# Optimization experiments

Measured on AMD Instinct MI355X. Metric: run time of the kernel, lower is better.

Reference implementation:

```python
import jax, jax.numpy as jnp
import numpy as np

T = 4        # number of atom types (len(atomtype))
N = 65536    # number of atoms
D = 256      # nl[0] == nl[1] == nl[2]
EPS = 1e-5   # LayerNorm eps (torch default)


def setup_inputs() -> dict:
    key = jax.random.key(0)
    ks = jax.random.split(key, 16)
    s = 1.0 / np.sqrt(D)  # xavier-ish scale
    f32 = jnp.float32
    return {
        "density": jax.random.normal(ks[0], (N, D), f32),
        "species": jax.random.randint(ks[1], (N,), 0, T, jnp.int32),
        # first Linear(nl[0], nl[1]) per type
        "W0": jax.random.normal(ks[2], (T, D, D), f32) * s,
        "b0": jnp.zeros((T, D), f32),
        # ResBlock: actfun (Relu_like: alpha*silu(Wx+b)), LayerNorm, Linear
        "Wa": jax.random.normal(ks[3], (T, D, D), f32) * s,
        "ba": jnp.zeros((T, D), f32),
        "alpha_a": jnp.ones((T, D), f32),
        "gamma": jnp.ones((T, D), f32),
        "beta_ln": jnp.zeros((T, D), f32),
        "Wl": jax.random.normal(ks[4], (T, D, D), f32) * s,
        "bl": jnp.zeros((T, D), f32),
        # tail actfun(nl[nhid-1], nl[nhid])
        "Wf": jax.random.normal(ks[5], (T, D, D), f32) * s,
        "bf": jnp.zeros((T, D), f32),
        "alpha_f": jnp.ones((T, D), f32),
        # output Linear(nl[nhid], outputneuron=1); randomized (zero-init is degenerate for testing)
        "Wo": jax.random.normal(ks[6], (T, 1, D), f32) * s,
        "bo": jnp.zeros((T, 1), f32),
    }


def _layernorm(x, g, b):
    mu = jnp.mean(x, axis=-1, keepdims=True)
    var = jnp.mean((x - mu) ** 2, axis=-1, keepdims=True)
    return g * (x - mu) * jax.lax.rsqrt(var + EPS) + b


def _expert(W0, b0, Wa, ba, alpha_a, gamma, beta_ln, Wl, bl, Wf, bf, alpha_f, Wo, bo, density):
    # Sequential: Linear -> ResBlock(actfun, LN, Linear) -> actfun -> Linear
    x = density @ W0.T + b0                       # [N, D]
    h = alpha_a * jax.nn.silu(x @ Wa.T + ba)      # Relu_like actfun
    h = _layernorm(h, gamma, beta_ln)
    x = x + (h @ Wl.T + bl)                       # residual add
    x = alpha_f * jax.nn.silu(x @ Wf.T + bf)
    return x @ Wo.T + bo                          # [N, 1]


def reference(density, species, W0, b0, Wa, ba, alpha_a, gamma, beta_ln, Wl, bl, Wf, bf, alpha_f, Wo, bo):
    # Apply every type's expert to all atoms, then pick the row for each atom's type.
    # Same math as the torch gather/scatter dispatch (every species value is in [0, T)).
    y_all = jax.vmap(_expert, in_axes=(0,) * 14 + (None,))(
        W0, b0, Wa, ba, alpha_a, gamma, beta_ln, Wl, bl, Wf, bf, alpha_f, Wo, bo, density
    )  # [T, N, 1]
    return y_all[species, jnp.arange(N)]          # [N, 1]
```

## Files before the change

### kernel.cpp

```cpp
#include <hip/hip_runtime.h>
#include <hip/hip_bf16.h>


#define D 256
#define T 4
#define MT 64
#define NTHREADS 512
#define CSTRIDE 32

#define XSW(row, col) (((row) << 8) + ((col) ^ (((row) & 7) << 3)))

typedef __attribute__((ext_vector_type(8))) short bf16x8;
typedef __attribute__((ext_vector_type(4))) float f32x4;

__device__ __forceinline__ float bf2f(unsigned short s) {
    union { unsigned u; float f; } c;
    c.u = ((unsigned)s) << 16;
    return c.f;
}
__device__ __forceinline__ unsigned cvtpk(float a, float b) {
    unsigned r;
    asm("v_cvt_pk_bf16_f32 %0, %1, %2" : "=v"(r) : "v"(a), "v"(b));
    return r;
}
__device__ __forceinline__ float lo2f(unsigned u) { return bf2f((unsigned short)(u & 0xffffu)); }
__device__ __forceinline__ float hi2f(unsigned u) { return bf2f((unsigned short)(u >> 16)); }
__device__ __forceinline__ float silu(float v) {
    return v * __builtin_amdgcn_rcpf(1.f + __expf(-v));
}

__device__ __forceinline__ void barrier_lds() {
    __builtin_amdgcn_sched_barrier(0);
    asm volatile("s_waitcnt lgkmcnt(0)" ::: "memory");
    __builtin_amdgcn_s_barrier();
    __builtin_amdgcn_sched_barrier(0);
}

extern "C" __global__ void k_prep(const int* __restrict__ species, int* cursors,
                                  int* __restrict__ perm, int N,
                                  const float* __restrict__ s0, const float* __restrict__ s1,
                                  const float* __restrict__ s2, const float* __restrict__ s3,
                                  unsigned short* __restrict__ d0, unsigned short* __restrict__ d1,
                                  unsigned short* __restrict__ d2, unsigned short* __restrict__ d3, int n4) {
    __shared__ int lh[T], lbase[T];
    int tid = threadIdx.x;
    if (tid < T) lh[tid] = 0;
    __syncthreads();
    int i = blockIdx.x * blockDim.x + tid;
    int t = -1, rank = 0;
    if (i < N) {
        t = species[i];
        rank = atomicAdd(&lh[t], 1);
    }
    if (i < n4) {
        float4 v;
        v = ((const float4*)s0)[i]; ((uint2*)d0)[i] = make_uint2(cvtpk(v.x, v.y), cvtpk(v.z, v.w));
        v = ((const float4*)s1)[i]; ((uint2*)d1)[i] = make_uint2(cvtpk(v.x, v.y), cvtpk(v.z, v.w));
        v = ((const float4*)s2)[i]; ((uint2*)d2)[i] = make_uint2(cvtpk(v.x, v.y), cvtpk(v.z, v.w));
        v = ((const float4*)s3)[i]; ((uint2*)d3)[i] = make_uint2(cvtpk(v.x, v.y), cvtpk(v.z, v.w));
    }
    __syncthreads();
    if (tid < T) lbase[tid] = atomicAdd(&cursors[tid * CSTRIDE], lh[tid]);
    __syncthreads();
    if (t >= 0) perm[t * N + lbase[t] + rank] = i;
}


extern "C" __global__ void __launch_bounds__(NTHREADS, 4)
fused_moe(const float* __restrict__ density,
          const int* __restrict__ perm,
          const int* __restrict__ counts,
          const unsigned short* __restrict__ W0b,
          const unsigned short* __restrict__ Wab,
          const unsigned short* __restrict__ Wlb,
          const unsigned short* __restrict__ Wfb,
          const float* __restrict__ b0g, const float* __restrict__ bag,
          const float* __restrict__ aag, const float* __restrict__ gg,
          const float* __restrict__ btg, const float* __restrict__ blg,
          const float* __restrict__ bfg, const float* __restrict__ afg,
          const float* __restrict__ Wog, const float* __restrict__ bog,
          float* __restrict__ out, int N)
{
    __shared__ unsigned short Xs[2][MT * D];
    __shared__ float Pb0[D], Pba[D], Paa[D], Pg[D], Pbt[D], Pbl[D], Pbf[D], Paf[D], Pwo[D];
    __shared__ float red1[NTHREADS], red2[NTHREADS];

    const int tid = threadIdx.x;

    const int nwg = gridDim.x;
    const int qq = nwg >> 3, rr = nwg & 7;
    const int xcd = blockIdx.x & 7, lid = blockIdx.x >> 3;
    const int vb = (xcd < rr ? xcd * (qq + 1) : rr * (qq + 1) + (xcd - rr) * qq) + lid;

    int c[T];
#pragma unroll
    for (int i = 0; i < T; ++i) c[i] = counts[i * CSTRIDE];
    int t = -1, tile = 0, rem = vb;
#pragma unroll
    for (int i = 0; i < T; ++i) {
        int ti = (c[i] + MT - 1) >> 6;
        if (t < 0) {
            if (rem < ti) { t = i; tile = rem; }
            else rem -= ti;
        }
    }
    if (t < 0) return;
    const int bstart = t * N + tile * MT;
    const int nrows = min(MT, c[t] - tile * MT);

    const int lane = tid & 63;
    const int w    = tid >> 6;
    const int ml   = lane & 15;
    const int qk   = (lane >> 4) * 8;
    const int qr   = (lane >> 4) * 4;

    const size_t wmat = (size_t)t * D * D;
    const unsigned short* W0t = W0b + wmat;
    const unsigned short* Wat = Wab + wmat;
    const unsigned short* Wlt = Wlb + wmat;
    const unsigned short* Wft = Wfb + wmat;

    bf16x8 abuf[2][4];
    auto prefA = [&](const unsigned short* __restrict__ W) {
#pragma unroll
        for (int p = 0; p < 2; ++p)
#pragma unroll
            for (int s = 0; s < 2; ++s)
#pragma unroll
                for (int mi = 0; mi < 2; ++mi)
                    abuf[p][s * 2 + mi] =
                        *(const bf16x8*)(W + (size_t)(w * 32 + mi * 16 + ml) * D + p * 64 + s * 32 + qk);
    };

    prefA(W0t);

    if (tid < D) {
        int j = t * D + tid;
        Pb0[tid] = b0g[j]; Pba[tid] = bag[j]; Paa[tid] = aag[j];
        Pg[tid]  = gg[j];  Pbt[tid] = btg[j]; Pbl[tid] = blg[j];
        Pbf[tid] = bfg[j]; Paf[tid] = afg[j]; Pwo[tid] = Wog[j];
    }

#pragma unroll
    for (int p = 0; p < 2; ++p) {
        int row = p * 32 + (tid >> 4);
        int cbase = (tid & 15) * 4;
        if (row < nrows) {
            const float* src = density + (size_t)perm[bstart + row] * D;
#pragma unroll
            for (int j = 0; j < 4; ++j) {
                int col = cbase + j * 64;
                float4 v = *(const float4*)(src + col);
                *(uint2*)(&Xs[0][XSW(row, col)]) = make_uint2(cvtpk(v.x, v.y), cvtpk(v.z, v.w));
            }
        } else {
#pragma unroll
            for (int j = 0; j < 4; ++j)
                *(uint2*)(&Xs[0][XSW(row, cbase + j * 64)]) = make_uint2(0u, 0u);
        }
    }
    barrier_lds();

    f32x4 acc[2][4];
    const f32x4 zero4 = {0.f, 0.f, 0.f, 0.f};

    auto do_gemm = [&](const unsigned short* __restrict__ W, const unsigned short* __restrict__ Xb) {
#pragma unroll
        for (int mi = 0; mi < 2; ++mi)
#pragma unroll
            for (int ni = 0; ni < 4; ++ni) acc[mi][ni] = zero4;
#pragma unroll
        for (int kp = 0; kp < 4; ++kp) {
            const int cur = kp & 1;
#pragma unroll
            for (int s = 0; s < 2; ++s) {
                const int k0 = kp * 64 + s * 32;
                bf16x8 b[4];
#pragma unroll
                for (int ni = 0; ni < 4; ++ni)
                    b[ni] = *(const bf16x8*)(Xb + XSW(ni * 16 + ml, k0 + qk));
#pragma unroll
                for (int mi = 0; mi < 2; ++mi)
#pragma unroll
                    for (int ni = 0; ni < 4; ++ni)
                        acc[mi][ni] = __builtin_amdgcn_mfma_f32_16x16x32_bf16(
                            abuf[cur][s * 2 + mi], b[ni], acc[mi][ni], 0, 0, 0);
                if (kp < 2) {
                    const int kb = (kp + 2) * 64 + s * 32;
#pragma unroll
                    for (int mi = 0; mi < 2; ++mi)
                        abuf[cur][s * 2 + mi] =
                            *(const bf16x8*)(W + (size_t)(w * 32 + mi * 16 + ml) * D + kb + qk);
                }
            }
        }
    };


    do_gemm(W0t, Xs[0]);
    prefA(Wat);
#pragma unroll
    for (int mi = 0; mi < 2; ++mi) {
#pragma unroll
        for (int ni = 0; ni < 4; ++ni) {
            int r0 = w * 32 + mi * 16 + qr;
            int a0 = ni * 16 + ml;
            float4 bb = *(const float4*)(Pb0 + r0);
            unsigned p01 = cvtpk(acc[mi][ni][0] + bb.x, acc[mi][ni][1] + bb.y);
            unsigned p23 = cvtpk(acc[mi][ni][2] + bb.z, acc[mi][ni][3] + bb.w);
            *(uint2*)(&Xs[1][XSW(a0, r0)]) = make_uint2(p01, p23);
        }
    }
    barrier_lds();

    do_gemm(Wat, Xs[1]);
    prefA(Wlt);
#pragma unroll
    for (int mi = 0; mi < 2; ++mi) {
#pragma unroll
        for (int ni = 0; ni < 4; ++ni) {
            int r0 = w * 32 + mi * 16 + qr;
            int a0 = ni * 16 + ml;
            float4 bb = *(const float4*)(Pba + r0);
            float4 aa = *(const float4*)(Paa + r0);
            float v0 = aa.x * silu(acc[mi][ni][0] + bb.x);
            float v1 = aa.y * silu(acc[mi][ni][1] + bb.y);
            float v2 = aa.z * silu(acc[mi][ni][2] + bb.z);
            float v3 = aa.w * silu(acc[mi][ni][3] + bb.w);
            *(uint2*)(&Xs[0][XSW(a0, r0)]) = make_uint2(cvtpk(v0, v1), cvtpk(v2, v3));
        }
    }
    barrier_lds();

    {
        int row = tid & 63, q = tid >> 6;
        bf16x8 hv[4];
        float sum = 0.f, ssq = 0.f;
#pragma unroll
        for (int j = 0; j < 4; ++j) {
            hv[j] = *(const bf16x8*)(&Xs[0][XSW(row, q * 32 + j * 8)]);
#pragma unroll
            for (int e = 0; e < 8; ++e) {
                float f = bf2f((unsigned short)hv[j][e]);
                sum += f;
                ssq = fmaf(f, f, ssq);
            }
        }
        red1[tid] = sum; red2[tid] = ssq;
        barrier_lds();
        if (tid < MT) {
            float s = 0.f, sq = 0.f;
#pragma unroll
            for (int k = 0; k < 8; ++k) { s += red1[tid + 64 * k]; sq += red2[tid + 64 * k]; }
            float mu = s * (1.f / D);
            float var = sq * (1.f / D) - mu * mu;
            red1[tid] = mu;
            red2[tid] = rsqrtf(var + 1e-5f);
        }
        barrier_lds();
        float mu = red1[row], rs = red2[row];
#pragma unroll
        for (int j = 0; j < 4; ++j) {
            float n[8];
#pragma unroll
            for (int e = 0; e < 8; ++e) {
                int col = q * 32 + j * 8 + e;
                float f = bf2f((unsigned short)hv[j][e]);
                n[e] = fmaf((f - mu) * rs, Pg[col], Pbt[col]);
            }
            uint4 o = make_uint4(cvtpk(n[0], n[1]), cvtpk(n[2], n[3]),
                                 cvtpk(n[4], n[5]), cvtpk(n[6], n[7]));
            *(uint4*)(&Xs[0][XSW(row, q * 32 + j * 8)]) = o;
        }
    }
    barrier_lds();

    do_gemm(Wlt, Xs[0]);
    prefA(Wft);
#pragma unroll
    for (int mi = 0; mi < 2; ++mi) {
#pragma unroll
        for (int ni = 0; ni < 4; ++ni) {
            int r0 = w * 32 + mi * 16 + qr;
            int a0 = ni * 16 + ml;
            float4 bb = *(const float4*)(Pbl + r0);
            uint2 old = *(const uint2*)(&Xs[1][XSW(a0, r0)]);
            float v0 = acc[mi][ni][0] + bb.x + lo2f(old.x);
            float v1 = acc[mi][ni][1] + bb.y + hi2f(old.x);
            float v2 = acc[mi][ni][2] + bb.z + lo2f(old.y);
            float v3 = acc[mi][ni][3] + bb.w + hi2f(old.y);
            *(uint2*)(&Xs[1][XSW(a0, r0)]) = make_uint2(cvtpk(v0, v1), cvtpk(v2, v3));
        }
    }
    barrier_lds();

    do_gemm(Wft, Xs[1]);
#pragma unroll
    for (int mi = 0; mi < 2; ++mi) {
#pragma unroll
        for (int ni = 0; ni < 4; ++ni) {
            int r0 = w * 32 + mi * 16 + qr;
            int a0 = ni * 16 + ml;
            float4 bb = *(const float4*)(Pbf + r0);
            float4 aa = *(const float4*)(Paf + r0);
            float v0 = aa.x * silu(acc[mi][ni][0] + bb.x);
            float v1 = aa.y * silu(acc[mi][ni][1] + bb.y);
            float v2 = aa.z * silu(acc[mi][ni][2] + bb.z);
            float v3 = aa.w * silu(acc[mi][ni][3] + bb.w);
            *(uint2*)(&Xs[0][XSW(a0, r0)]) = make_uint2(cvtpk(v0, v1), cvtpk(v2, v3));
        }
    }
    barrier_lds();

    {
        int row = tid & 63, q = tid >> 6;
        float part = 0.f;
#pragma unroll
        for (int j = 0; j < 4; ++j) {
            bf16x8 hv = *(const bf16x8*)(&Xs[0][XSW(row, q * 32 + j * 8)]);
#pragma unroll
            for (int e = 0; e < 8; ++e)
                part = fmaf(bf2f((unsigned short)hv[e]), Pwo[q * 32 + j * 8 + e], part);
        }
        red1[tid] = part;
        barrier_lds();
        if (tid < nrows) {
            float val = bog[t];
#pragma unroll
            for (int k = 0; k < 8; ++k) val += red1[tid + 64 * k];
            out[perm[bstart + tid]] = val;
        }
    }
}


extern "C" void kernel_launch(void* const* d_in, const int* in_sizes, int n_in,
                              void* d_out, int out_size, void* d_ws, size_t ws_size,
                              hipStream_t stream) {
    const float* density = (const float*)d_in[0];
    const int*   species = (const int*)d_in[1];
    const float* W0      = (const float*)d_in[2];
    const float* b0      = (const float*)d_in[3];
    const float* Wa      = (const float*)d_in[4];
    const float* ba      = (const float*)d_in[5];
    const float* alpha_a = (const float*)d_in[6];
    const float* gamma   = (const float*)d_in[7];
    const float* beta_ln = (const float*)d_in[8];
    const float* Wl      = (const float*)d_in[9];
    const float* bl      = (const float*)d_in[10];
    const float* Wf      = (const float*)d_in[11];
    const float* bfv     = (const float*)d_in[12];
    const float* alpha_f = (const float*)d_in[13];
    const float* Wo      = (const float*)d_in[14];
    const float* bo      = (const float*)d_in[15];
    float* out = (float*)d_out;
    const int N = in_sizes[1];

    char* ws = (char*)d_ws;
    int* cursors = (int*)ws;
    int* perm    = (int*)(ws + 1024);
    const size_t wsz = (size_t)T * D * D;
    unsigned short* W0b = (unsigned short*)(ws + 1024 + (size_t)T * N * 4);
    unsigned short* Wab = W0b + wsz;
    unsigned short* Wlb = Wab + wsz;
    unsigned short* Wfb = Wlb + wsz;

    hipMemsetAsync(ws, 0, 512, stream);
    int n4 = (int)(wsz / 4);
    int pb = ((N > n4 ? N : n4) + 255) / 256;
    k_prep<<<pb, 256, 0, stream>>>(species, cursors, perm, N, W0, Wa, Wl, Wf,
                                   W0b, Wab, Wlb, Wfb, n4);

    int nblocks = (N + MT - 1) / MT + T;
    fused_moe<<<nblocks, NTHREADS, 0, stream>>>(density, perm, cursors, W0b, Wab, Wlb, Wfb,
                                                b0, ba, alpha_a, gamma, beta_ln, bl, bfv, alpha_f,
                                                Wo, bo, out, N);
}
```

Measured before the change: 195.0 us.

## Fuse LayerNorm stats and output dot into GEMM epilogues, drop A-prefetch

Computes the LayerNorm sum and sum-of-squares directly from fp32 accumulators in the second GEMM epilogue, reducing them with wave shuffles and a small LDS array. The separate LDS pass that re-read the activations for statistics goes away. The final silu and output dot product are likewise fused into the last GEMM epilogue, which removes one LDS write, a barrier and a read. The double-buffered register prefetch of weight tiles is replaced by a simple per-k load. That lowers register pressure but exposes global or L2 latency inside the GEMM loop.

```diff
diff --git a/kernel.cpp b/kernel.cpp
--- a/kernel.cpp
+++ b/kernel.cpp
@@ -120,20 +120,6 @@
     const unsigned short* Wlt = Wlb + wmat;
     const unsigned short* Wft = Wfb + wmat;
 
-    bf16x8 abuf[2][4];
-    auto prefA = [&](const unsigned short* __restrict__ W) {
-#pragma unroll
-        for (int p = 0; p < 2; ++p)
-#pragma unroll
-            for (int s = 0; s < 2; ++s)
-#pragma unroll
-                for (int mi = 0; mi < 2; ++mi)
-                    abuf[p][s * 2 + mi] =
-                        *(const bf16x8*)(W + (size_t)(w * 32 + mi * 16 + ml) * D + p * 64 + s * 32 + qk);
-    };
-
-    prefA(W0t);
-
     if (tid < D) {
         int j = t * D + tid;
         Pb0[tid] = b0g[j]; Pba[tid] = bag[j]; Paa[tid] = aag[j];
@@ -170,35 +156,25 @@
 #pragma unroll
             for (int ni = 0; ni < 4; ++ni) acc[mi][ni] = zero4;
 #pragma unroll
-        for (int kp = 0; kp < 4; ++kp) {
-            const int cur = kp & 1;
-#pragma unroll
-            for (int s = 0; s < 2; ++s) {
-                const int k0 = kp * 64 + s * 32;
-                bf16x8 b[4];
+        for (int k0 = 0; k0 < D; k0 += 32) {
+            bf16x8 a[2], b[4];
+#pragma unroll
+            for (int mi = 0; mi < 2; ++mi)
+                a[mi] = *(const bf16x8*)(W + (size_t)(w * 32 + mi * 16 + ml) * D + k0 + qk);
+#pragma unroll
+            for (int ni = 0; ni < 4; ++ni)
+                b[ni] = *(const bf16x8*)(Xb + XSW(ni * 16 + ml, k0 + qk));
+#pragma unroll
+            for (int mi = 0; mi < 2; ++mi)
 #pragma unroll
                 for (int ni = 0; ni < 4; ++ni)
-                    b[ni] = *(const bf16x8*)(Xb + XSW(ni * 16 + ml, k0 + qk));
-#pragma unroll
-                for (int mi = 0; mi < 2; ++mi)
-#pragma unroll
-                    for (int ni = 0; ni < 4; ++ni)
-                        acc[mi][ni] = __builtin_amdgcn_mfma_f32_16x16x32_bf16(
-                            abuf[cur][s * 2 + mi], b[ni], acc[mi][ni], 0, 0, 0);
-                if (kp < 2) {
-                    const int kb = (kp + 2) * 64 + s * 32;
-#pragma unroll
-                    for (int mi = 0; mi < 2; ++mi)
-                        abuf[cur][s * 2 + mi] =
-                            *(const bf16x8*)(W + (size_t)(w * 32 + mi * 16 + ml) * D + kb + qk);
-                }
-            }
+                    acc[mi][ni] = __builtin_amdgcn_mfma_f32_16x16x32_bf16(
+                        a[mi], b[ni], acc[mi][ni], 0, 0, 0);
         }
     };
 
 
     do_gemm(W0t, Xs[0]);
-    prefA(Wat);
 #pragma unroll
     for (int mi = 0; mi < 2; ++mi) {
 #pragma unroll
@@ -214,58 +190,64 @@
     barrier_lds();
 
     do_gemm(Wat, Xs[1]);
-    prefA(Wlt);
-#pragma unroll
-    for (int mi = 0; mi < 2; ++mi) {
+    {
+        float psum[4] = {0.f, 0.f, 0.f, 0.f}, pssq[4] = {0.f, 0.f, 0.f, 0.f};
+#pragma unroll
+        for (int mi = 0; mi < 2; ++mi) {
+#pragma unroll
+            for (int ni = 0; ni < 4; ++ni) {
+                int r0 = w * 32 + mi * 16 + qr;
+                int a0 = ni * 16 + ml;
+                float4 bb = *(const float4*)(Pba + r0);
+                float4 aa = *(const float4*)(Paa + r0);
+                float v0 = aa.x * silu(acc[mi][ni][0] + bb.x);
+                float v1 = aa.y * silu(acc[mi][ni][1] + bb.y);
+                float v2 = aa.z * silu(acc[mi][ni][2] + bb.z);
+                float v3 = aa.w * silu(acc[mi][ni][3] + bb.w);
+                psum[ni] += v0 + v1 + v2 + v3;
+                pssq[ni] = fmaf(v0, v0, fmaf(v1, v1, fmaf(v2, v2, fmaf(v3, v3, pssq[ni]))));
+                *(uint2*)(&Xs[0][XSW(a0, r0)]) = make_uint2(cvtpk(v0, v1), cvtpk(v2, v3));
+            }
+        }
 #pragma unroll
         for (int ni = 0; ni < 4; ++ni) {
-            int r0 = w * 32 + mi * 16 + qr;
-            int a0 = ni * 16 + ml;
-            float4 bb = *(const float4*)(Pba + r0);
-            float4 aa = *(const float4*)(Paa + r0);
-            float v0 = aa.x * silu(acc[mi][ni][0] + bb.x);
-            float v1 = aa.y * silu(acc[mi][ni][1] + bb.y);
-            float v2 = aa.z * silu(acc[mi][ni][2] + bb.z);
-            float v3 = aa.w * silu(acc[mi][ni][3] + bb.w);
-            *(uint2*)(&Xs[0][XSW(a0, r0)]) = make_uint2(cvtpk(v0, v1), cvtpk(v2, v3));
-        }
-    }
-    barrier_lds();
-
+            psum[ni] += __shfl_xor(psum[ni], 16, 64);
+            psum[ni] += __shfl_xor(psum[ni], 32, 64);
+            pssq[ni] += __shfl_xor(pssq[ni], 16, 64);
+            pssq[ni] += __shfl_xor(pssq[ni], 32, 64);
+        }
+        if (lane < 16) {
+#pragma unroll
+            for (int ni = 0; ni < 4; ++ni) {
+                int a0 = ni * 16 + lane;
+                red1[a0 * 8 + w] = psum[ni];
+                red2[a0 * 8 + w] = pssq[ni];
+            }
+        }
+    }
+    barrier_lds();
+
+    if (tid < MT) {
+        float s = 0.f, sq = 0.f;
+#pragma unroll
+        for (int k = 0; k < 8; ++k) { s += red1[tid * 8 + k]; sq += red2[tid * 8 + k]; }
+        float mu = s * (1.f / D);
+        float var = sq * (1.f / D) - mu * mu;
+        red1[tid] = mu;
+        red2[tid] = rsqrtf(var + 1e-5f);
+    }
+    barrier_lds();
     {
         int row = tid & 63, q = tid >> 6;
-        bf16x8 hv[4];
-        float sum = 0.f, ssq = 0.f;
+        float mu = red1[row], rs = red2[row];
 #pragma unroll
         for (int j = 0; j < 4; ++j) {
-            hv[j] = *(const bf16x8*)(&Xs[0][XSW(row, q * 32 + j * 8)]);
-#pragma unroll
-            for (int e = 0; e < 8; ++e) {
-                float f = bf2f((unsigned short)hv[j][e]);
-                sum += f;
-                ssq = fmaf(f, f, ssq);
-            }
-        }
-        red1[tid] = sum; red2[tid] = ssq;
-        barrier_lds();
-        if (tid < MT) {
-            float s = 0.f, sq = 0.f;
-#pragma unroll
-            for (int k = 0; k < 8; ++k) { s += red1[tid + 64 * k]; sq += red2[tid + 64 * k]; }
-            float mu = s * (1.f / D);
-            float var = sq * (1.f / D) - mu * mu;
-            red1[tid] = mu;
-            red2[tid] = rsqrtf(var + 1e-5f);
-        }
-        barrier_lds();
-        float mu = red1[row], rs = red2[row];
-#pragma unroll
-        for (int j = 0; j < 4; ++j) {
+            bf16x8 hv = *(const bf16x8*)(&Xs[0][XSW(row, q * 32 + j * 8)]);
             float n[8];
 #pragma unroll
             for (int e = 0; e < 8; ++e) {
                 int col = q * 32 + j * 8 + e;
-                float f = bf2f((unsigned short)hv[j][e]);
+                float f = bf2f((unsigned short)hv[e]);
                 n[e] = fmaf((f - mu) * rs, Pg[col], Pbt[col]);
             }
             uint4 o = make_uint4(cvtpk(n[0], n[1]), cvtpk(n[2], n[3]),
@@ -276,7 +258,6 @@
     barrier_lds();
 
     do_gemm(Wlt, Xs[0]);
-    prefA(Wft);
 #pragma unroll
     for (int mi = 0; mi < 2; ++mi) {
 #pragma unroll
@@ -295,41 +276,41 @@
     barrier_lds();
 
     do_gemm(Wft, Xs[1]);
-#pragma unroll
-    for (int mi = 0; mi < 2; ++mi) {
+    {
+        float pdot[4] = {0.f, 0.f, 0.f, 0.f};
+#pragma unroll
+        for (int mi = 0; mi < 2; ++mi) {
+#pragma unroll
+            for (int ni = 0; ni < 4; ++ni) {
+                int r0 = w * 32 + mi * 16 + qr;
+                float4 bb = *(const float4*)(Pbf + r0);
+                float4 aa = *(const float4*)(Paf + r0);
+                float4 wo = *(const float4*)(Pwo + r0);
+                float v0 = aa.x * silu(acc[mi][ni][0] + bb.x);
+                float v1 = aa.y * silu(acc[mi][ni][1] + bb.y);
+                float v2 = aa.z * silu(acc[mi][ni][2] + bb.z);
+                float v3 = aa.w * silu(acc[mi][ni][3] + bb.w);
+                pdot[ni] = fmaf(v0, wo.x, fmaf(v1, wo.y, fmaf(v2, wo.z, fmaf(v3, wo.w, pdot[ni]))));
+            }
+        }
 #pragma unroll
         for (int ni = 0; ni < 4; ++ni) {
-            int r0 = w * 32 + mi * 16 + qr;
-            int a0 = ni * 16 + ml;
-            float4 bb = *(const float4*)(Pbf + r0);
-            float4 aa = *(const float4*)(Paf + r0);
-            float v0 = aa.x * silu(acc[mi][ni][0] + bb.x);
-            float v1 = aa.y * silu(acc[mi][ni][1] + bb.y);
-            float v2 = aa.z * silu(acc[mi][ni][2] + bb.z);
-            float v3 = aa.w * silu(acc[mi][ni][3] + bb.w);
-            *(uint2*)(&Xs[0][XSW(a0, r0)]) = make_uint2(cvtpk(v0, v1), cvtpk(v2, v3));
-        }
-    }
-    barrier_lds();
-
-    {
-        int row = tid & 63, q = tid >> 6;
-        float part = 0.f;
-#pragma unroll
-        for (int j = 0; j < 4; ++j) {
-            bf16x8 hv = *(const bf16x8*)(&Xs[0][XSW(row, q * 32 + j * 8)]);
-#pragma unroll
-            for (int e = 0; e < 8; ++e)
-                part = fmaf(bf2f((unsigned short)hv[e]), Pwo[q * 32 + j * 8 + e], part);
-        }
-        red1[tid] = part;
-        barrier_lds();
-        if (tid < nrows) {
-            float val = bog[t];
-#pragma unroll
-            for (int k = 0; k < 8; ++k) val += red1[tid + 64 * k];
-            out[perm[bstart + tid]] = val;
-        }
+            pdot[ni] += __shfl_xor(pdot[ni], 16, 64);
+            pdot[ni] += __shfl_xor(pdot[ni], 32, 64);
+        }
+        if (lane < 16) {
+#pragma unroll
+            for (int ni = 0; ni < 4; ++ni)
+                red1[(ni * 16 + lane) * 8 + w] = pdot[ni];
+        }
+    }
+    barrier_lds();
+
+    if (tid < nrows) {
+        float val = bog[t];
+#pragma unroll
+        for (int k = 0; k < 8; ++k) val += red1[tid * 8 + k];
+        out[perm[bstart + tid]] = val;
     }
 }
 
```

Result: slower. 202.7 us (+3.9%).

## Halve row tile to 32 and drop weight register prefetch for higher occupancy

Applied to the files above, without the earlier changes.

The atom tile per block is halved from 64 to 32 rows, so each warp computes a 32x32 output block per GEMM instead of 32x64. The double-buffered register prefetch of weight fragments is removed; weights are now loaded directly inside the k-loop. Launch bounds are raised to allow 6 blocks per CU. The LayerNorm and output-reduction thread mappings are reworked to 16 threads per row. The intent is more blocks and waves in flight to hide latency, at the cost of reading each weight matrix twice as often per atom and losing the explicit global-load overlap.

```diff
diff --git a/kernel.cpp b/kernel.cpp
--- a/kernel.cpp
+++ b/kernel.cpp
@@ -4,7 +4,7 @@
 
 #define D 256
 #define T 4
-#define MT 64
+#define MT 32
 #define NTHREADS 512
 #define CSTRIDE 32
 
@@ -66,7 +66,7 @@
 }
 
 
-extern "C" __global__ void __launch_bounds__(NTHREADS, 4)
+extern "C" __global__ void __launch_bounds__(NTHREADS, 6)
 fused_moe(const float* __restrict__ density,
           const int* __restrict__ perm,
           const int* __restrict__ counts,
@@ -98,7 +98,7 @@
     int t = -1, tile = 0, rem = vb;
 #pragma unroll
     for (int i = 0; i < T; ++i) {
-        int ti = (c[i] + MT - 1) >> 6;
+        int ti = (c[i] + MT - 1) >> 5;
         if (t < 0) {
             if (rem < ti) { t = i; tile = rem; }
             else rem -= ti;
@@ -120,20 +120,6 @@
     const unsigned short* Wlt = Wlb + wmat;
     const unsigned short* Wft = Wfb + wmat;
 
-    bf16x8 abuf[2][4];
-    auto prefA = [&](const unsigned short* __restrict__ W) {
-#pragma unroll
-        for (int p = 0; p < 2; ++p)
-#pragma unroll
-            for (int s = 0; s < 2; ++s)
-#pragma unroll
-                for (int mi = 0; mi < 2; ++mi)
-                    abuf[p][s * 2 + mi] =
-                        *(const bf16x8*)(W + (size_t)(w * 32 + mi * 16 + ml) * D + p * 64 + s * 32 + qk);
-    };
-
-    prefA(W0t);
-
     if (tid < D) {
         int j = t * D + tid;
         Pb0[tid] = b0g[j]; Pba[tid] = bag[j]; Paa[tid] = aag[j];
@@ -141,9 +127,8 @@
         Pbf[tid] = bfg[j]; Paf[tid] = afg[j]; Pwo[tid] = Wog[j];
     }
 
-#pragma unroll
-    for (int p = 0; p < 2; ++p) {
-        int row = p * 32 + (tid >> 4);
+    {
+        int row = tid >> 4;
         int cbase = (tid & 15) * 4;
         if (row < nrows) {
             const float* src = density + (size_t)perm[bstart + row] * D;
@@ -161,48 +146,38 @@
     }
     barrier_lds();
 
-    f32x4 acc[2][4];
+    f32x4 acc[2][2];
     const f32x4 zero4 = {0.f, 0.f, 0.f, 0.f};
 
     auto do_gemm = [&](const unsigned short* __restrict__ W, const unsigned short* __restrict__ Xb) {
 #pragma unroll
         for (int mi = 0; mi < 2; ++mi)
 #pragma unroll
-            for (int ni = 0; ni < 4; ++ni) acc[mi][ni] = zero4;
-#pragma unroll
-        for (int kp = 0; kp < 4; ++kp) {
-            const int cur = kp & 1;
-#pragma unroll
-            for (int s = 0; s < 2; ++s) {
-                const int k0 = kp * 64 + s * 32;
-                bf16x8 b[4];
-#pragma unroll
-                for (int ni = 0; ni < 4; ++ni)
-                    b[ni] = *(const bf16x8*)(Xb + XSW(ni * 16 + ml, k0 + qk));
-#pragma unroll
-                for (int mi = 0; mi < 2; ++mi)
-#pragma unroll
-                    for (int ni = 0; ni < 4; ++ni)
-                        acc[mi][ni] = __builtin_amdgcn_mfma_f32_16x16x32_bf16(
-                            abuf[cur][s * 2 + mi], b[ni], acc[mi][ni], 0, 0, 0);
-                if (kp < 2) {
-                    const int kb = (kp + 2) * 64 + s * 32;
-#pragma unroll
-                    for (int mi = 0; mi < 2; ++mi)
-                        abuf[cur][s * 2 + mi] =
-                            *(const bf16x8*)(W + (size_t)(w * 32 + mi * 16 + ml) * D + kb + qk);
-                }
-            }
+            for (int ni = 0; ni < 2; ++ni) acc[mi][ni] = zero4;
+#pragma unroll
+        for (int k0 = 0; k0 < D; k0 += 32) {
+            bf16x8 a[2], b[2];
+#pragma unroll
+            for (int mi = 0; mi < 2; ++mi)
+                a[mi] = *(const bf16x8*)(W + (size_t)(w * 32 + mi * 16 + ml) * D + k0 + qk);
+#pragma unroll
+            for (int ni = 0; ni < 2; ++ni)
+                b[ni] = *(const bf16x8*)(Xb + XSW(ni * 16 + ml, k0 + qk));
+#pragma unroll
+            for (int mi = 0; mi < 2; ++mi)
+#pragma unroll
+                for (int ni = 0; ni < 2; ++ni)
+                    acc[mi][ni] = __builtin_amdgcn_mfma_f32_16x16x32_bf16(
+                        a[mi], b[ni], acc[mi][ni], 0, 0, 0);
         }
     };
 
 
     do_gemm(W0t, Xs[0]);
-    prefA(Wat);
 #pragma unroll
     for (int mi = 0; mi < 2; ++mi) {
 #pragma unroll
-        for (int ni = 0; ni < 4; ++ni) {
+        for (int ni = 0; ni < 2; ++ni) {
             int r0 = w * 32 + mi * 16 + qr;
             int a0 = ni * 16 + ml;
             float4 bb = *(const float4*)(Pb0 + r0);
@@ -214,11 +189,10 @@
     barrier_lds();
 
     do_gemm(Wat, Xs[1]);
-    prefA(Wlt);
 #pragma unroll
     for (int mi = 0; mi < 2; ++mi) {
 #pragma unroll
-        for (int ni = 0; ni < 4; ++ni) {
+        for (int ni = 0; ni < 2; ++ni) {
             int r0 = w * 32 + mi * 16 + qr;
             int a0 = ni * 16 + ml;
             float4 bb = *(const float4*)(Pba + r0);
@@ -233,12 +207,13 @@
     barrier_lds();
 
     {
-        int row = tid & 63, q = tid >> 6;
-        bf16x8 hv[4];
+        int row = tid >> 4, sub = tid & 15;
+        int col0 = sub * 16;
+        bf16x8 hv[2];
         float sum = 0.f, ssq = 0.f;
 #pragma unroll
-        for (int j = 0; j < 4; ++j) {
-            hv[j] = *(const bf16x8*)(&Xs[0][XSW(row, q * 32 + j * 8)]);
+        for (int j = 0; j < 2; ++j) {
+            hv[j] = *(const bf16x8*)(&Xs[0][XSW(row, col0 + j * 8)]);
 #pragma unroll
             for (int e = 0; e < 8; ++e) {
                 float f = bf2f((unsigned short)hv[j][e]);
@@ -251,7 +226,7 @@
         if (tid < MT) {
             float s = 0.f, sq = 0.f;
 #pragma unroll
-            for (int k = 0; k < 8; ++k) { s += red1[tid + 64 * k]; sq += red2[tid + 64 * k]; }
+            for (int k = 0; k < 16; ++k) { s += red1[tid * 16 + k]; sq += red2[tid * 16 + k]; }
             float mu = s * (1.f / D);
             float var = sq * (1.f / D) - mu * mu;
             red1[tid] = mu;
@@ -260,27 +235,27 @@
         barrier_lds();
         float mu = red1[row], rs = red2[row];
 #pragma unroll
-        for (int j = 0; j < 4; ++j) {
+        for (int j = 0; j < 2; ++j) {
             float n[8];
 #pragma unroll
             for (int e = 0; e < 8; ++e) {
-                int col = q * 32 + j * 8 + e;
+                int col = col0 + j * 8 + e;
                 float f = bf2f((unsigned short)hv[j][e]);
                 n[e] = fmaf((f - mu) * rs, Pg[col], Pbt[col]);
             }
-            uint4 o = make_uint4(cvtpk(n[0], n[1]), cvtpk(n[2], n[3]),
-                                 cvtpk(n[4], n[5]), cvtpk(n[6], n[7]));
-            *(uint4*)(&Xs[0][XSW(row, q * 32 + j * 8)]) = o;
+            uint2 o = make_uint2(cvtpk(n[0], n[1]), cvtpk(n[2], n[3]));
+            uint2 o2 = make_uint2(cvtpk(n[4], n[5]), cvtpk(n[6], n[7]));
+            *(uint2*)(&Xs[0][XSW(row, col0 + j * 8)]) = o;
+            *(uint2*)(&Xs[0][XSW(row, col0 + j * 8 + 4)]) = o2;
         }
     }
     barrier_lds();
 
     do_gemm(Wlt, Xs[0]);
-    prefA(Wft);
 #pragma unroll
     for (int mi = 0; mi < 2; ++mi) {
 #pragma unroll
-        for (int ni = 0; ni < 4; ++ni) {
+        for (int ni = 0; ni < 2; ++ni) {
             int r0 = w * 32 + mi * 16 + qr;
             int a0 = ni * 16 + ml;
             float4 bb = *(const float4*)(Pbl + r0);
@@ -298,7 +273,7 @@
 #pragma unroll
     for (int mi = 0; mi < 2; ++mi) {
 #pragma unroll
-        for (int ni = 0; ni < 4; ++ni) {
+        for (int ni = 0; ni < 2; ++ni) {
             int r0 = w * 32 + mi * 16 + qr;
             int a0 = ni * 16 + ml;
             float4 bb = *(const float4*)(Pbf + r0);
@@ -313,21 +288,22 @@
     barrier_lds();
 
     {
-        int row = tid & 63, q = tid >> 6;
+        int row = tid >> 4, sub = tid & 15;
+        int col0 = sub * 16;
         float part = 0.f;
 #pragma unroll
-        for (int j = 0; j < 4; ++j) {
-            bf16x8 hv = *(const bf16x8*)(&Xs[0][XSW(row, q * 32 + j * 8)]);
+        for (int j = 0; j < 2; ++j) {
+            bf16x8 hv = *(const bf16x8*)(&Xs[0][XSW(row, col0 + j * 8)]);
 #pragma unroll
             for (int e = 0; e < 8; ++e)
-                part = fmaf(bf2f((unsigned short)hv[e]), Pwo[q * 32 + j * 8 + e], part);
+                part = fmaf(bf2f((unsigned short)hv[e]), Pwo[col0 + j * 8 + e], part);
         }
         red1[tid] = part;
         barrier_lds();
         if (tid < nrows) {
             float val = bog[t];
 #pragma unroll
-            for (int k = 0; k < 8; ++k) val += red1[tid + 64 * k];
+            for (int k = 0; k < 16; ++k) val += red1[tid * 16 + k];
             out[perm[bstart + tid]] = val;
         }
     }
```

Result: slower. 248.7 us (+27.5%).
